# Performance work log

Measured on AMD Instinct MI355X. Metric: run time of the kernel, lower is better.

## Reference

```python
import jax, jax.numpy as jnp
import numpy as np

S, B, E, H = 2048, 4, 512, 8
HD = E // H


def setup_inputs() -> dict:
    key = jax.random.key(0)
    ks = jax.random.split(key, 5)
    scale = 1.0 / np.sqrt(E)
    return {
        "query": jax.random.normal(ks[0], (S, B, E), jnp.float32),
        "key": jax.random.normal(ks[1], (S, B, E), jnp.float32),
        "value": jax.random.normal(ks[2], (S, B, E), jnp.float32),
        "in_proj_weight": jax.random.normal(ks[3], (3 * E, E), jnp.float32) * scale,
        "in_proj_bias": jnp.zeros((3 * E,), jnp.float32),
        "out_proj_weight": jax.random.normal(ks[4], (E, E), jnp.float32) * scale,
        "out_proj_bias": jnp.zeros((E,), jnp.float32),
    }


def reference(query, key, value, in_proj_weight, in_proj_bias, out_proj_weight, out_proj_bias):
    tgt_len, bsz, embed_dim = query.shape
    src_len = key.shape[0]
    # Quirk of this module: first chunk (w_qk) projects BOTH q and k; third chunk projects v.
    w_qk = in_proj_weight[:embed_dim]
    w_v = in_proj_weight[2 * embed_dim:]
    b_qk = in_proj_bias[:embed_dim]
    b_v = in_proj_bias[2 * embed_dim:]
    q = query @ w_qk.T + b_qk          # [S, B, E]
    k = key @ w_qk.T + b_qk
    v = value @ w_v.T + b_v
    # (S, B, E) -> (B*H, S, HD)
    def split_heads(x, n):
        return x.reshape(n, bsz * H, HD).transpose(1, 0, 2)
    q = split_heads(q, tgt_len) / jnp.sqrt(jnp.asarray(HD, q.dtype))
    k = split_heads(k, src_len)
    v = split_heads(v, src_len)
    scores = jnp.einsum("bqd,bkd->bqk", q, k)          # [B*H, S, S] full score matrix
    attn = jax.nn.softmax(scores, axis=-1)
    out = jnp.einsum("bqk,bkd->bqd", attn, v)          # [B*H, S, HD]
    out = out.transpose(1, 0, 2).reshape(tgt_len * bsz, embed_dim)
    out = out @ out_proj_weight.T + out_proj_bias
    return out.reshape(tgt_len, bsz, embed_dim)
```

## Files before the change

kernel.cpp:

```cpp
#include <hip/hip_runtime.h>
#include <hip/hip_bf16.h>

typedef __attribute__((ext_vector_type(8))) short s16x8;
typedef __attribute__((ext_vector_type(4))) short s16x4;
typedef __attribute__((ext_vector_type(4))) float f32x4;

#if __has_builtin(__builtin_amdgcn_exp2f)
#define EXP2F(x) __builtin_amdgcn_exp2f(x)
#else
#define EXP2F(x) exp2f(x)
#endif

#define S_LEN 2048
#define EMB   512
#define MROWS 8192

__device__ __forceinline__ float bf2f(short x) {
    union { float f; unsigned u; } z; z.u = ((unsigned)(unsigned short)x) << 16; return z.f;
}
__device__ __forceinline__ short f2bf(float f) {
    union { float f; unsigned u; } z; z.f = f;
    unsigned r = z.u + 0x7FFF + ((z.u >> 16) & 1);
    return (short)(r >> 16);
}
__device__ __forceinline__ short f2bf_fast(float f) {
    union { float f; unsigned u; } z; z.f = f;
    return (short)((z.u + 0x8000u) >> 16);
}

template<int AF32, int BF32>
__device__ __forceinline__ void gemm_mainloop(const void* __restrict__ Ag,
                                              const void* __restrict__ Bg,
                                              short* sA, short* sB,
                                              f32x4 acc[2][4], int K)
{
    const int tid  = threadIdx.x;
    const int lane = tid & 63;
    const int wv   = tid >> 6;
    const int l15  = lane & 15, quad = lane >> 4;
    const int wm   = (wv >> 1) * 32, wn = (wv & 1) * 64;

    f32x4 afr[2], bfr[2];
    s16x8 ahr, bhr;

    auto loadT = [&](const void* G, int kt, f32x4* fr, s16x8& hr, int F32) {
        if (F32) {
#pragma unroll
            for (int p = 0; p < 2; ++p) {
                int c = tid + p * 512;
                fr[p] = *(const f32x4*)((const float*)G + (size_t)(c >> 3) * K + kt + (c & 7) * 4);
            }
        } else {
            hr = *(const s16x8*)((const short*)G + (size_t)(tid >> 2) * K + kt + (tid & 3) * 8);
        }
    };
    auto commitT = [&](short* s, f32x4* fr, s16x8& hr, int F32) {
        if (F32) {
#pragma unroll
            for (int p = 0; p < 2; ++p) {
                int c = tid + p * 512;
                s16x4 o4;
                o4[0] = f2bf_fast(fr[p][0]); o4[1] = f2bf_fast(fr[p][1]);
                o4[2] = f2bf_fast(fr[p][2]); o4[3] = f2bf_fast(fr[p][3]);
                *(s16x4*)(s + c * 4) = o4;
            }
        } else {
            *(s16x8*)(s + tid * 8) = hr;
        }
    };

    loadT(Ag, 0, afr, ahr, AF32);
    loadT(Bg, 0, bfr, bhr, BF32);
    commitT(sA, afr, ahr, AF32);
    commitT(sB, bfr, bhr, BF32);
    __syncthreads();

    int cur = 0;
    for (int kt = 0; kt < K; kt += 32) {
        const int ktn = (kt + 32 < K) ? kt + 32 : 0;
        loadT(Ag, ktn, afr, ahr, AF32);
        loadT(Bg, ktn, bfr, bhr, BF32);

        const short* sAc = sA + cur * 4096;
        const short* sBc = sB + cur * 4096;
        s16x8 aF[2], bF[4];
#pragma unroll
        for (int i = 0; i < 2; ++i)
            aF[i] = *(const s16x8*)(sAc + (wm + i * 16 + l15) * 32 + quad * 8);
#pragma unroll
        for (int j = 0; j < 4; ++j)
            bF[j] = *(const s16x8*)(sBc + (wn + j * 16 + l15) * 32 + quad * 8);
#pragma unroll
        for (int i = 0; i < 2; ++i)
#pragma unroll
            for (int j = 0; j < 4; ++j)
                acc[i][j] = __builtin_amdgcn_mfma_f32_16x16x32_bf16(aF[i], bF[j], acc[i][j], 0, 0, 0);

        commitT(sA + (cur ^ 1) * 4096, afr, ahr, AF32);
        commitT(sB + (cur ^ 1) * 4096, bfr, bhr, BF32);
        __syncthreads();
        cur ^= 1;
    }
}

__global__ __launch_bounds__(512, 4) void qkv_proj(const float* __restrict__ query,
                                                   const float* __restrict__ key,
                                                   const float* __restrict__ value,
                                                   const float* __restrict__ W,
                                                   const float* __restrict__ bias,
                                                   short* __restrict__ q,
                                                   short* __restrict__ k,
                                                   short* __restrict__ vt)
{
    __shared__ __align__(16) short smem[16384];
    short* sA = smem;
    short* sB = smem + 8192;

    const int z = blockIdx.z;
    const float* X  = (z == 0) ? query : (z == 1) ? key : value;
    const float* Wz = W    + (z == 2 ? (size_t)1024 * EMB : 0);
    const float* bz = bias + (z == 2 ? 1024 : 0);
    const float scale = (z == 0) ? 0.125f * 1.44269504f : 1.0f;

    const int blockM = blockIdx.x * 128, blockN = blockIdx.y * 128;

    f32x4 acc[2][4];
#pragma unroll
    for (int i = 0; i < 2; ++i)
#pragma unroll
        for (int j = 0; j < 4; ++j)
            acc[i][j] = (f32x4){0.f, 0.f, 0.f, 0.f};

    gemm_mainloop<1, 1>(X + (size_t)blockM * EMB, Wz + (size_t)blockN * EMB,
                        sA, sB, acc, EMB);

    const int tid = threadIdx.x, lane = tid & 63, wv = tid >> 6;
    const int l15 = lane & 15, quad = lane >> 4;
    const int wm = (wv >> 1) * 32, wn = (wv & 1) * 64;

#pragma unroll
    for (int j = 0; j < 4; ++j) {
        int colL = wn + j * 16 + l15;
        float bval = bz[blockN + colL];
        int hL = colL >> 6, hd = colL & 63;
#pragma unroll
        for (int i = 0; i < 2; ++i) {
#pragma unroll
            for (int r = 0; r < 4; ++r) {
                int rowL = wm + i * 16 + quad * 4 + r;
                int b = rowL & 3, sp = rowL >> 2;
                float val = (acc[i][j][r] + bval) * scale;
                int idx = (z == 2) ? (((b * 2 + hL) * 64 + hd) * 32 + sp)
                                   : (((b * 2 + hL) * 32 + sp) * 64 + hd);
                smem[idx] = f2bf(val);
            }
        }
    }
    __syncthreads();

    const s16x8* src = (const s16x8*)(smem + tid * 32);
    if (z == 2) {
        int b = tid >> 7, hL = (tid >> 6) & 1, hd = tid & 63;
        int h = (blockN >> 6) + hL;
        short* dst = vt + ((size_t)(b * 8 + h) * 64 + hd) * 2048 + (blockM >> 2);
#pragma unroll
        for (int u = 0; u < 4; ++u) ((s16x8*)dst)[u] = src[u];
    } else {
        int b = tid >> 7, hL = (tid >> 6) & 1;
        int sp = (tid >> 1) & 31, hdh = (tid & 1) * 32;
        int h = (blockN >> 6) + hL;
        short* dstp = (z == 0) ? q : k;
        short* dst = dstp + ((size_t)(b * 8 + h) * 2048 + (blockM >> 2) + sp) * 64 + hdh;
#pragma unroll
        for (int u = 0; u < 4; ++u) ((s16x8*)dst)[u] = src[u];
    }
}

__global__ __launch_bounds__(256, 2) void flash_attn(const short* __restrict__ q,
                                                     const short* __restrict__ k,
                                                     const short* __restrict__ vt,
                                                     short* __restrict__ attn)
{
    __shared__ __align__(16) short sK[2][64 * 72];
    __shared__ __align__(16) short sV[2][64 * 72];
    const int bh = blockIdx.x;
    const int q0 = blockIdx.y * 128;
    const int tid = threadIdx.x, wv = tid >> 6, lane = tid & 63;
    const int l15 = lane & 15, quad = lane >> 4;

    s16x8 qf[2][2];
#pragma unroll
    for (int qr = 0; qr < 2; ++qr) {
        const short* qp = q + ((size_t)(bh * 2048 + q0 + wv * 32 + qr * 16 + l15)) * 64 + quad * 8;
        qf[qr][0] = *(const s16x8*)qp;
        qf[qr][1] = *(const s16x8*)(qp + 32);
    }

    const short* kg = k  + (size_t)bh * 2048 * 64;
    const short* vg = vt + (size_t)bh * 64 * 2048;

    const int r0 = tid >> 3,          c0 = (tid & 7) * 8;
    const int r1 = (tid + 256) >> 3,  c1 = ((tid + 256) & 7) * 8;
    const int p0 = (r0 & 35) | ((r0 & 24) >> 1) | ((r0 & 4) << 2);
    const int p1 = (r1 & 35) | ((r1 & 24) >> 1) | ((r1 & 4) << 2);

    f32x4 o[2][4];
    float ls[2][4];
#pragma unroll
    for (int qr = 0; qr < 2; ++qr)
#pragma unroll
        for (int i = 0; i < 4; ++i) { o[qr][i] = (f32x4){0.f, 0.f, 0.f, 0.f}; ls[qr][i] = 0.f; }

    s16x8 ka = *(const s16x8*)(kg + (size_t)r0 * 64 + c0);
    s16x8 kb = *(const s16x8*)(kg + (size_t)r1 * 64 + c1);
    s16x8 va = *(const s16x8*)(vg + (size_t)r0 * 2048 + c0);
    s16x8 vb = *(const s16x8*)(vg + (size_t)r1 * 2048 + c1);
    *(s16x8*)(sK[0] + p0 * 72 + c0) = ka;
    *(s16x8*)(sK[0] + p1 * 72 + c1) = kb;
    *(s16x8*)(sV[0] + r0 * 72 + c0) = va;
    *(s16x8*)(sV[0] + r1 * 72 + c1) = vb;
    __syncthreads();

    int cur = 0;
    for (int kt = 0; kt < 2048; kt += 64) {
        const int ktn = (kt + 64) & 2047;
        ka = *(const s16x8*)(kg + (size_t)(ktn + r0) * 64 + c0);
        kb = *(const s16x8*)(kg + (size_t)(ktn + r1) * 64 + c1);
        va = *(const s16x8*)(vg + (size_t)r0 * 2048 + ktn + c0);
        vb = *(const s16x8*)(vg + (size_t)r1 * 2048 + ktn + c1);

        const short* Kc = sK[cur];
        const short* Vc = sV[cur];

        f32x4 sc[2][4];
#pragma unroll
        for (int ct = 0; ct < 4; ++ct) {
            s16x8 kf0 = *(const s16x8*)(Kc + (ct * 16 + l15) * 72 + quad * 8);
            s16x8 kf1 = *(const s16x8*)(Kc + (ct * 16 + l15) * 72 + quad * 8 + 32);
#pragma unroll
            for (int qr = 0; qr < 2; ++qr) {
                f32x4 c = (f32x4){0.f, 0.f, 0.f, 0.f};
                c = __builtin_amdgcn_mfma_f32_16x16x32_bf16(kf0, qf[qr][0], c, 0, 0, 0);
                c = __builtin_amdgcn_mfma_f32_16x16x32_bf16(kf1, qf[qr][1], c, 0, 0, 0);
                sc[qr][ct] = c;
            }
        }
        s16x8 pf[2][2];
#pragma unroll
        for (int qr = 0; qr < 2; ++qr)
#pragma unroll
            for (int c = 0; c < 2; ++c)
#pragma unroll
                for (int h = 0; h < 2; ++h)
#pragma unroll
                    for (int r = 0; r < 4; ++r) {
                        float p = EXP2F(sc[qr][2 * c + h][r]);
                        ls[qr][r] += p;
                        pf[qr][c][h * 4 + r] = f2bf_fast(p);
                    }
#pragma unroll
        for (int nt = 0; nt < 4; ++nt)
#pragma unroll
            for (int c = 0; c < 2; ++c) {
                s16x8 vf = *(const s16x8*)(Vc + (nt * 16 + l15) * 72 + c * 32 + quad * 8);
#pragma unroll
                for (int qr = 0; qr < 2; ++qr)
                    o[qr][nt] = __builtin_amdgcn_mfma_f32_16x16x32_bf16(pf[qr][c], vf, o[qr][nt], 0, 0, 0);
            }
        short* Kn = sK[cur ^ 1];
        short* Vn = sV[cur ^ 1];
        *(s16x8*)(Kn + p0 * 72 + c0) = ka;
        *(s16x8*)(Kn + p1 * 72 + c1) = kb;
        *(s16x8*)(Vn + r0 * 72 + c0) = va;
        *(s16x8*)(Vn + r1 * 72 + c1) = vb;
        __syncthreads();
        cur ^= 1;
    }

    const int b = bh >> 3, h = bh & 7;
#pragma unroll
    for (int qr = 0; qr < 2; ++qr) {
        float s = ls[qr][0] + ls[qr][1] + ls[qr][2] + ls[qr][3];
        s += __shfl_xor(s, 16, 64);
        s += __shfl_xor(s, 32, 64);
        float sinv = 1.0f / s;
        float inv[4];
#pragma unroll
        for (int r = 0; r < 4; ++r)
            inv[r] = __shfl(sinv, quad * 20 + r, 64);
#pragma unroll
        for (int r = 0; r < 4; ++r) {
            int srow = q0 + wv * 32 + qr * 16 + quad * 4 + r;
#pragma unroll
            for (int nt = 0; nt < 4; ++nt)
                attn[(size_t)(srow * 4 + b) * 512 + h * 64 + nt * 16 + l15] = f2bf(o[qr][nt][r] * inv[r]);
        }
    }
}

__global__ __launch_bounds__(512, 4) void out_proj(const short* __restrict__ attn,
                                                   const float* __restrict__ W,
                                                   const float* __restrict__ bias,
                                                   float* __restrict__ out)
{
    __shared__ __align__(16) short sA[2 * 4096], sB[2 * 4096];
    const int blockM = blockIdx.x * 128, blockN = blockIdx.y * 128;

    f32x4 acc[2][4];
#pragma unroll
    for (int i = 0; i < 2; ++i)
#pragma unroll
        for (int j = 0; j < 4; ++j)
            acc[i][j] = (f32x4){0.f, 0.f, 0.f, 0.f};

    gemm_mainloop<0, 1>(attn + (size_t)blockM * EMB, W + (size_t)blockN * EMB,
                        sA, sB, acc, EMB);

    const int tid = threadIdx.x, lane = tid & 63, wv = tid >> 6;
    const int l15 = lane & 15, quad = lane >> 4;
    const int wm = (wv >> 1) * 32, wn = (wv & 1) * 64;

#pragma unroll
    for (int j = 0; j < 4; ++j) {
        int col = blockN + wn + j * 16 + l15;
        float bval = bias[col];
#pragma unroll
        for (int i = 0; i < 2; ++i) {
#pragma unroll
            for (int r = 0; r < 4; ++r) {
                int row = blockM + wm + i * 16 + quad * 4 + r;
                out[(size_t)row * 512 + col] = acc[i][j][r] + bval;
            }
        }
    }
}

extern "C" void kernel_launch(void* const* d_in, const int* in_sizes, int n_in,
                              void* d_out, int out_size, void* d_ws, size_t ws_size,
                              hipStream_t stream)
{
    const float* query = (const float*)d_in[0];
    const float* key   = (const float*)d_in[1];
    const float* value = (const float*)d_in[2];
    const float* ipw   = (const float*)d_in[3];
    const float* ipb   = (const float*)d_in[4];
    const float* opw   = (const float*)d_in[5];
    const float* opb   = (const float*)d_in[6];
    float* out = (float*)d_out;

    const size_t NELEM = (size_t)MROWS * EMB;
    short* q    = (short*)d_ws;
    short* k    = q + NELEM;
    short* attn = k + NELEM;
    short* vt   = (short*)d_out;

    qkv_proj  <<<dim3(64, 4, 3), 512, 0, stream>>>(query, key, value, ipw, ipb, q, k, vt);
    flash_attn<<<dim3(32, 16),   256, 0, stream>>>(q, k, vt, attn);
    out_proj  <<<dim3(64, 4),    512, 0, stream>>>(attn, opw, opb, out);
}
```

Baseline: 188.0 us.

## Pre-convert weights to bf16 and store LDS tiles in MFMA fragment order

Adds a small kernel that converts the input projection weight to bf16 once per call, so the QKV GEMM reads half the bytes for its B operand and skips per-tile conversion. The GEMM and flash-attention staging are reorganised so each thread writes LDS data already in MFMA fragment order. Fragment reads then become contiguous 16-byte per-lane loads with no padding or swizzle arithmetic. The cost is an extra kernel launch, and the weight copy lives in scratch space carved from the output buffer.

After: 204.9 us. 9.0% more time.

```diff
diff --git a/kernel.cpp b/kernel.cpp
--- a/kernel.cpp
+++ b/kernel.cpp
@@ -28,6 +28,20 @@
     return (short)((z.u + 0x8000u) >> 16);
 }
 
+__global__ __launch_bounds__(256) void w_to_bf16(const float* __restrict__ W,
+                                                 short* __restrict__ wb, int n)
+{
+    int i = (blockIdx.x * 256 + threadIdx.x) * 8;
+    if (i < n) {
+        f32x4 a = *(const f32x4*)(W + i);
+        f32x4 b = *(const f32x4*)(W + i + 4);
+        s16x8 o;
+        o[0] = f2bf(a[0]); o[1] = f2bf(a[1]); o[2] = f2bf(a[2]); o[3] = f2bf(a[3]);
+        o[4] = f2bf(b[0]); o[5] = f2bf(b[1]); o[6] = f2bf(b[2]); o[7] = f2bf(b[3]);
+        *(s16x8*)(wb + i) = o;
+    }
+}
+
 template<int AF32, int BF32>
 __device__ __forceinline__ void gemm_mainloop(const void* __restrict__ Ag,
                                               const void* __restrict__ Bg,
@@ -37,33 +51,33 @@
     const int tid  = threadIdx.x;
     const int lane = tid & 63;
     const int wv   = tid >> 6;
-    const int l15  = lane & 15, quad = lane >> 4;
-    const int wm   = (wv >> 1) * 32, wn = (wv & 1) * 64;
+
+    const int srow = (tid >> 6) * 16 + (tid & 15);
+    const int scol = ((tid >> 4) & 3) * 8;
+
+    const int amt = (wv >> 1) * 2;
+    const int bnt = (wv & 1) * 4;
 
     f32x4 afr[2], bfr[2];
     s16x8 ahr, bhr;
 
     auto loadT = [&](const void* G, int kt, f32x4* fr, s16x8& hr, int F32) {
         if (F32) {
-#pragma unroll
-            for (int p = 0; p < 2; ++p) {
-                int c = tid + p * 512;
-                fr[p] = *(const f32x4*)((const float*)G + (size_t)(c >> 3) * K + kt + (c & 7) * 4);
-            }
+            const float* g = (const float*)G + (size_t)srow * K + kt + scol;
+            fr[0] = *(const f32x4*)g;
+            fr[1] = *(const f32x4*)(g + 4);
         } else {
-            hr = *(const s16x8*)((const short*)G + (size_t)(tid >> 2) * K + kt + (tid & 3) * 8);
+            hr = *(const s16x8*)((const short*)G + (size_t)srow * K + kt + scol);
         }
     };
     auto commitT = [&](short* s, f32x4* fr, s16x8& hr, int F32) {
         if (F32) {
-#pragma unroll
-            for (int p = 0; p < 2; ++p) {
-                int c = tid + p * 512;
-                s16x4 o4;
-                o4[0] = f2bf_fast(fr[p][0]); o4[1] = f2bf_fast(fr[p][1]);
-                o4[2] = f2bf_fast(fr[p][2]); o4[3] = f2bf_fast(fr[p][3]);
-                *(s16x4*)(s + c * 4) = o4;
-            }
+            s16x8 o;
+            o[0] = f2bf_fast(fr[0][0]); o[1] = f2bf_fast(fr[0][1]);
+            o[2] = f2bf_fast(fr[0][2]); o[3] = f2bf_fast(fr[0][3]);
+            o[4] = f2bf_fast(fr[1][0]); o[5] = f2bf_fast(fr[1][1]);
+            o[6] = f2bf_fast(fr[1][2]); o[7] = f2bf_fast(fr[1][3]);
+            *(s16x8*)(s + tid * 8) = o;
         } else {
             *(s16x8*)(s + tid * 8) = hr;
         }
@@ -86,10 +100,10 @@
         s16x8 aF[2], bF[4];
 #pragma unroll
         for (int i = 0; i < 2; ++i)
-            aF[i] = *(const s16x8*)(sAc + (wm + i * 16 + l15) * 32 + quad * 8);
+            aF[i] = *(const s16x8*)(sAc + ((amt + i) * 64 + lane) * 8);
 #pragma unroll
         for (int j = 0; j < 4; ++j)
-            bF[j] = *(const s16x8*)(sBc + (wn + j * 16 + l15) * 32 + quad * 8);
+            bF[j] = *(const s16x8*)(sBc + ((bnt + j) * 64 + lane) * 8);
 #pragma unroll
         for (int i = 0; i < 2; ++i)
 #pragma unroll
@@ -106,7 +120,7 @@
 __global__ __launch_bounds__(512, 4) void qkv_proj(const float* __restrict__ query,
                                                    const float* __restrict__ key,
                                                    const float* __restrict__ value,
-                                                   const float* __restrict__ W,
+                                                   const short* __restrict__ wb,
                                                    const float* __restrict__ bias,
                                                    short* __restrict__ q,
                                                    short* __restrict__ k,
@@ -118,7 +132,7 @@
 
     const int z = blockIdx.z;
     const float* X  = (z == 0) ? query : (z == 1) ? key : value;
-    const float* Wz = W    + (z == 2 ? (size_t)1024 * EMB : 0);
+    const short* Wz = wb   + (z == 2 ? (size_t)1024 * EMB : 0);
     const float* bz = bias + (z == 2 ? 1024 : 0);
     const float scale = (z == 0) ? 0.125f * 1.44269504f : 1.0f;
 
@@ -131,7 +145,7 @@
         for (int j = 0; j < 4; ++j)
             acc[i][j] = (f32x4){0.f, 0.f, 0.f, 0.f};
 
-    gemm_mainloop<1, 1>(X + (size_t)blockM * EMB, Wz + (size_t)blockN * EMB,
+    gemm_mainloop<1, 0>(X + (size_t)blockM * EMB, Wz + (size_t)blockN * EMB,
                         sA, sB, acc, EMB);
 
     const int tid = threadIdx.x, lane = tid & 63, wv = tid >> 6;
@@ -181,8 +195,8 @@
                                                      const short* __restrict__ vt,
                                                      short* __restrict__ attn)
 {
-    __shared__ __align__(16) short sK[2][64 * 72];
-    __shared__ __align__(16) short sV[2][64 * 72];
+    __shared__ __align__(16) short sK[2][4096];
+    __shared__ __align__(16) short sV[2][4096];
     const int bh = blockIdx.x;
     const int q0 = blockIdx.y * 128;
     const int tid = threadIdx.x, wv = tid >> 6, lane = tid & 63;
@@ -199,10 +213,14 @@
     const short* kg = k  + (size_t)bh * 2048 * 64;
     const short* vg = vt + (size_t)bh * 64 * 2048;
 
-    const int r0 = tid >> 3,          c0 = (tid & 7) * 8;
-    const int r1 = (tid + 256) >> 3,  c1 = ((tid + 256) & 7) * 8;
-    const int p0 = (r0 & 35) | ((r0 & 24) >> 1) | ((r0 & 4) << 2);
-    const int p1 = (r1 & 35) | ((r1 & 24) >> 1) | ((r1 & 4) << 2);
+    const int l15s = tid & 15;
+    const int qs   = (tid >> 4) & 3;
+    const int cts  = tid >> 6;
+    const int pr   = cts * 16 + l15s;
+    const int rK   = (pr & 35) | ((pr & 12) << 1) | ((pr & 16) >> 2);
+    const int hdV  = cts * 16 + l15s;
+    const short* kgt = kg + (size_t)rK * 64 + qs * 8;
+    const short* vgt = vg + (size_t)hdV * 2048 + qs * 8;
 
     f32x4 o[2][4];
     float ls[2][4];
@@ -211,23 +229,23 @@
 #pragma unroll
         for (int i = 0; i < 4; ++i) { o[qr][i] = (f32x4){0.f, 0.f, 0.f, 0.f}; ls[qr][i] = 0.f; }
 
-    s16x8 ka = *(const s16x8*)(kg + (size_t)r0 * 64 + c0);
-    s16x8 kb = *(const s16x8*)(kg + (size_t)r1 * 64 + c1);
-    s16x8 va = *(const s16x8*)(vg + (size_t)r0 * 2048 + c0);
-    s16x8 vb = *(const s16x8*)(vg + (size_t)r1 * 2048 + c1);
-    *(s16x8*)(sK[0] + p0 * 72 + c0) = ka;
-    *(s16x8*)(sK[0] + p1 * 72 + c1) = kb;
-    *(s16x8*)(sV[0] + r0 * 72 + c0) = va;
-    *(s16x8*)(sV[0] + r1 * 72 + c1) = vb;
+    s16x8 ka = *(const s16x8*)(kgt);
+    s16x8 kb = *(const s16x8*)(kgt + 32);
+    s16x8 va = *(const s16x8*)(vgt);
+    s16x8 vb = *(const s16x8*)(vgt + 32);
+    *(s16x8*)(sK[0] + tid * 8)        = ka;
+    *(s16x8*)(sK[0] + 2048 + tid * 8) = kb;
+    *(s16x8*)(sV[0] + tid * 8)        = va;
+    *(s16x8*)(sV[0] + 2048 + tid * 8) = vb;
     __syncthreads();
 
     int cur = 0;
     for (int kt = 0; kt < 2048; kt += 64) {
         const int ktn = (kt + 64) & 2047;
-        ka = *(const s16x8*)(kg + (size_t)(ktn + r0) * 64 + c0);
-        kb = *(const s16x8*)(kg + (size_t)(ktn + r1) * 64 + c1);
-        va = *(const s16x8*)(vg + (size_t)r0 * 2048 + ktn + c0);
-        vb = *(const s16x8*)(vg + (size_t)r1 * 2048 + ktn + c1);
+        ka = *(const s16x8*)(kgt + (size_t)ktn * 64);
+        kb = *(const s16x8*)(kgt + (size_t)ktn * 64 + 32);
+        va = *(const s16x8*)(vgt + ktn);
+        vb = *(const s16x8*)(vgt + ktn + 32);
 
         const short* Kc = sK[cur];
         const short* Vc = sV[cur];
@@ -235,8 +253,8 @@
         f32x4 sc[2][4];
 #pragma unroll
         for (int ct = 0; ct < 4; ++ct) {
-            s16x8 kf0 = *(const s16x8*)(Kc + (ct * 16 + l15) * 72 + quad * 8);
-            s16x8 kf1 = *(const s16x8*)(Kc + (ct * 16 + l15) * 72 + quad * 8 + 32);
+            s16x8 kf0 = *(const s16x8*)(Kc + (ct * 64 + lane) * 8);
+            s16x8 kf1 = *(const s16x8*)(Kc + (ct * 64 + lane) * 8 + 2048);
 #pragma unroll
             for (int qr = 0; qr < 2; ++qr) {
                 f32x4 c = (f32x4){0.f, 0.f, 0.f, 0.f};
@@ -262,17 +280,15 @@
         for (int nt = 0; nt < 4; ++nt)
 #pragma unroll
             for (int c = 0; c < 2; ++c) {
-                s16x8 vf = *(const s16x8*)(Vc + (nt * 16 + l15) * 72 + c * 32 + quad * 8);
+                s16x8 vf = *(const s16x8*)(Vc + ((c * 4 + nt) * 64 + lane) * 8);
 #pragma unroll
                 for (int qr = 0; qr < 2; ++qr)
                     o[qr][nt] = __builtin_amdgcn_mfma_f32_16x16x32_bf16(pf[qr][c], vf, o[qr][nt], 0, 0, 0);
             }
-        short* Kn = sK[cur ^ 1];
-        short* Vn = sV[cur ^ 1];
-        *(s16x8*)(Kn + p0 * 72 + c0) = ka;
-        *(s16x8*)(Kn + p1 * 72 + c1) = kb;
-        *(s16x8*)(Vn + r0 * 72 + c0) = va;
-        *(s16x8*)(Vn + r1 * 72 + c1) = vb;
+        *(s16x8*)(sK[cur ^ 1] + tid * 8)        = ka;
+        *(s16x8*)(sK[cur ^ 1] + 2048 + tid * 8) = kb;
+        *(s16x8*)(sV[cur ^ 1] + tid * 8)        = va;
+        *(s16x8*)(sV[cur ^ 1] + 2048 + tid * 8) = vb;
         __syncthreads();
         cur ^= 1;
     }
@@ -353,8 +369,10 @@
     short* k    = q + NELEM;
     short* attn = k + NELEM;
     short* vt   = (short*)d_out;
-
-    qkv_proj  <<<dim3(64, 4, 3), 512, 0, stream>>>(query, key, value, ipw, ipb, q, k, vt);
+    short* wb   = (short*)d_out + NELEM;
+
+    w_to_bf16 <<<dim3(384),      256, 0, stream>>>(ipw, wb, 1536 * EMB);
+    qkv_proj  <<<dim3(64, 4, 3), 512, 0, stream>>>(query, key, value, wb, ipb, q, k, vt);
     flash_attn<<<dim3(32, 16),   256, 0, stream>>>(q, k, vt, attn);
     out_proj  <<<dim3(64, 4),    512, 0, stream>>>(attn, opw, opb, out);
 }
```

## Swizzle LDS layouts into MFMA fragment order to avoid bank conflicts

Applied to the files above, without the earlier changes.

Shared-memory tiles in the projection GEMM mainloop and the flash-attention K/V buffers are re-laid out in MFMA fragment order with an XOR swizzle, so each lane reads its 16-byte fragment at a contiguous swizzled offset instead of a padded row-major stride. The V-transpose staging buffer in the QKV epilogue also gets an XOR swizzle on its column chunks. The aim is to remove LDS bank conflicts on fragment reads and writes, and in attention to drop the padding, which shrinks LDS use. Global load patterns change as well (fewer rows per thread, two strided chunks), which may affect coalescing.

Result: slower. 202.9 us (+7.9%).

```diff
diff --git a/kernel.cpp b/kernel.cpp
--- a/kernel.cpp
+++ b/kernel.cpp
@@ -15,9 +15,6 @@
 #define EMB   512
 #define MROWS 8192
 
-__device__ __forceinline__ float bf2f(short x) {
-    union { float f; unsigned u; } z; z.u = ((unsigned)(unsigned short)x) << 16; return z.f;
-}
 __device__ __forceinline__ short f2bf(float f) {
     union { float f; unsigned u; } z; z.f = f;
     unsigned r = z.u + 0x7FFF + ((z.u >> 16) & 1);
@@ -27,6 +24,7 @@
     union { float f; unsigned u; } z; z.f = f;
     return (short)((z.u + 0x8000u) >> 16);
 }
+__device__ __forceinline__ int swzs(int s) { return s ^ ((s >> 3) & 7); }
 
 template<int AF32, int BF32>
 __device__ __forceinline__ void gemm_mainloop(const void* __restrict__ Ag,
@@ -37,35 +35,39 @@
     const int tid  = threadIdx.x;
     const int lane = tid & 63;
     const int wv   = tid >> 6;
-    const int l15  = lane & 15, quad = lane >> 4;
-    const int wm   = (wv >> 1) * 32, wn = (wv & 1) * 64;
+    const int lsw  = lane ^ ((lane >> 3) & 7);
+    const int amt  = (wv >> 1) * 2;
+    const int bnt  = (wv & 1) * 4;
+
+    const int brow = tid >> 2, bqd = tid & 3;
+    const int boff = swzs((brow >> 4) * 64 + bqd * 16 + (brow & 15)) * 8;
+    const int frow = tid >> 3, ffc = tid & 7;
+    const int foff = swzs((frow >> 4) * 64 + (ffc >> 1) * 16 + (frow & 15)) * 8
+                   + (ffc & 1) * 4;
 
     f32x4 afr[2], bfr[2];
     s16x8 ahr, bhr;
 
     auto loadT = [&](const void* G, int kt, f32x4* fr, s16x8& hr, int F32) {
         if (F32) {
-#pragma unroll
-            for (int p = 0; p < 2; ++p) {
-                int c = tid + p * 512;
-                fr[p] = *(const f32x4*)((const float*)G + (size_t)(c >> 3) * K + kt + (c & 7) * 4);
-            }
+            const float* g = (const float*)G + (size_t)frow * K + kt + ffc * 4;
+            fr[0] = *(const f32x4*)g;
+            fr[1] = *(const f32x4*)(g + (size_t)64 * K);
         } else {
-            hr = *(const s16x8*)((const short*)G + (size_t)(tid >> 2) * K + kt + (tid & 3) * 8);
+            hr = *(const s16x8*)((const short*)G + (size_t)brow * K + kt + bqd * 8);
         }
     };
     auto commitT = [&](short* s, f32x4* fr, s16x8& hr, int F32) {
         if (F32) {
 #pragma unroll
             for (int p = 0; p < 2; ++p) {
-                int c = tid + p * 512;
                 s16x4 o4;
                 o4[0] = f2bf_fast(fr[p][0]); o4[1] = f2bf_fast(fr[p][1]);
                 o4[2] = f2bf_fast(fr[p][2]); o4[3] = f2bf_fast(fr[p][3]);
-                *(s16x4*)(s + c * 4) = o4;
+                *(s16x4*)(s + foff + p * 2048) = o4;
             }
         } else {
-            *(s16x8*)(s + tid * 8) = hr;
+            *(s16x8*)(s + boff) = hr;
         }
     };
 
@@ -86,10 +88,10 @@
         s16x8 aF[2], bF[4];
 #pragma unroll
         for (int i = 0; i < 2; ++i)
-            aF[i] = *(const s16x8*)(sAc + (wm + i * 16 + l15) * 32 + quad * 8);
+            aF[i] = *(const s16x8*)(sAc + ((amt + i) * 64 + lsw) * 8);
 #pragma unroll
         for (int j = 0; j < 4; ++j)
-            bF[j] = *(const s16x8*)(sBc + (wn + j * 16 + l15) * 32 + quad * 8);
+            bF[j] = *(const s16x8*)(sBc + ((bnt + j) * 64 + lsw) * 8);
 #pragma unroll
         for (int i = 0; i < 2; ++i)
 #pragma unroll
@@ -150,22 +152,29 @@
                 int rowL = wm + i * 16 + quad * 4 + r;
                 int b = rowL & 3, sp = rowL >> 2;
                 float val = (acc[i][j][r] + bval) * scale;
-                int idx = (z == 2) ? (((b * 2 + hL) * 64 + hd) * 32 + sp)
-                                   : (((b * 2 + hL) * 32 + sp) * 64 + hd);
+                int idx;
+                if (z == 2) {
+                    int R = (b * 2 + hL) * 64 + hd;
+                    idx = R * 32 + (((sp >> 3) ^ (R & 3)) << 3) + (sp & 7);
+                } else {
+                    idx = ((b * 2 + hL) * 32 + sp) * 64 + hd;
+                }
                 smem[idx] = f2bf(val);
             }
         }
     }
     __syncthreads();
 
-    const s16x8* src = (const s16x8*)(smem + tid * 32);
     if (z == 2) {
+        int R = tid;
         int b = tid >> 7, hL = (tid >> 6) & 1, hd = tid & 63;
         int h = (blockN >> 6) + hL;
         short* dst = vt + ((size_t)(b * 8 + h) * 64 + hd) * 2048 + (blockM >> 2);
 #pragma unroll
-        for (int u = 0; u < 4; ++u) ((s16x8*)dst)[u] = src[u];
+        for (int u = 0; u < 4; ++u)
+            ((s16x8*)dst)[u] = *(const s16x8*)(smem + R * 32 + ((u ^ (R & 3)) << 3));
     } else {
+        const s16x8* src = (const s16x8*)(smem + tid * 32);
         int b = tid >> 7, hL = (tid >> 6) & 1;
         int sp = (tid >> 1) & 31, hdh = (tid & 1) * 32;
         int h = (blockN >> 6) + hL;
@@ -181,12 +190,13 @@
                                                      const short* __restrict__ vt,
                                                      short* __restrict__ attn)
 {
-    __shared__ __align__(16) short sK[2][64 * 72];
-    __shared__ __align__(16) short sV[2][64 * 72];
+    __shared__ __align__(16) short sK[2][4096];
+    __shared__ __align__(16) short sV[2][4096];
     const int bh = blockIdx.x;
     const int q0 = blockIdx.y * 128;
     const int tid = threadIdx.x, wv = tid >> 6, lane = tid & 63;
     const int l15 = lane & 15, quad = lane >> 4;
+    const int lsw = lane ^ ((lane >> 3) & 7);
 
     s16x8 qf[2][2];
 #pragma unroll
@@ -199,10 +209,12 @@
     const short* kg = k  + (size_t)bh * 2048 * 64;
     const short* vg = vt + (size_t)bh * 64 * 2048;
 
-    const int r0 = tid >> 3,          c0 = (tid & 7) * 8;
-    const int r1 = (tid + 256) >> 3,  c1 = ((tid + 256) & 7) * 8;
-    const int p0 = (r0 & 35) | ((r0 & 24) >> 1) | ((r0 & 4) << 2);
-    const int p1 = (r1 & 35) | ((r1 & 24) >> 1) | ((r1 & 4) << 2);
+    const int rk = tid >> 2, qd = tid & 3;
+    const int pr = (rk & 35) | ((rk & 24) >> 1) | ((rk & 4) << 2);
+    const int kw0 = swzs((pr >> 4) * 64 + qd * 16 + (pr & 15)) * 8;
+    const int vw0 = swzs((rk >> 4) * 64 + qd * 16 + (rk & 15)) * 8;
+    const short* kgt = kg + (size_t)rk * 64 + qd * 8;
+    const short* vgt = vg + (size_t)rk * 2048 + qd * 8;
 
     f32x4 o[2][4];
     float ls[2][4];
@@ -211,23 +223,23 @@
 #pragma unroll
         for (int i = 0; i < 4; ++i) { o[qr][i] = (f32x4){0.f, 0.f, 0.f, 0.f}; ls[qr][i] = 0.f; }
 
-    s16x8 ka = *(const s16x8*)(kg + (size_t)r0 * 64 + c0);
-    s16x8 kb = *(const s16x8*)(kg + (size_t)r1 * 64 + c1);
-    s16x8 va = *(const s16x8*)(vg + (size_t)r0 * 2048 + c0);
-    s16x8 vb = *(const s16x8*)(vg + (size_t)r1 * 2048 + c1);
-    *(s16x8*)(sK[0] + p0 * 72 + c0) = ka;
-    *(s16x8*)(sK[0] + p1 * 72 + c1) = kb;
-    *(s16x8*)(sV[0] + r0 * 72 + c0) = va;
-    *(s16x8*)(sV[0] + r1 * 72 + c1) = vb;
+    s16x8 ka = *(const s16x8*)(kgt);
+    s16x8 kb = *(const s16x8*)(kgt + 32);
+    s16x8 va = *(const s16x8*)(vgt);
+    s16x8 vb = *(const s16x8*)(vgt + 32);
+    *(s16x8*)(sK[0] + kw0)        = ka;
+    *(s16x8*)(sK[0] + kw0 + 2048) = kb;
+    *(s16x8*)(sV[0] + vw0)        = va;
+    *(s16x8*)(sV[0] + vw0 + 2048) = vb;
     __syncthreads();
 
     int cur = 0;
     for (int kt = 0; kt < 2048; kt += 64) {
         const int ktn = (kt + 64) & 2047;
-        ka = *(const s16x8*)(kg + (size_t)(ktn + r0) * 64 + c0);
-        kb = *(const s16x8*)(kg + (size_t)(ktn + r1) * 64 + c1);
-        va = *(const s16x8*)(vg + (size_t)r0 * 2048 + ktn + c0);
-        vb = *(const s16x8*)(vg + (size_t)r1 * 2048 + ktn + c1);
+        ka = *(const s16x8*)(kgt + (size_t)ktn * 64);
+        kb = *(const s16x8*)(kgt + (size_t)ktn * 64 + 32);
+        va = *(const s16x8*)(vgt + ktn);
+        vb = *(const s16x8*)(vgt + ktn + 32);
 
         const short* Kc = sK[cur];
         const short* Vc = sV[cur];
@@ -235,8 +247,8 @@
         f32x4 sc[2][4];
 #pragma unroll
         for (int ct = 0; ct < 4; ++ct) {
-            s16x8 kf0 = *(const s16x8*)(Kc + (ct * 16 + l15) * 72 + quad * 8);
-            s16x8 kf1 = *(const s16x8*)(Kc + (ct * 16 + l15) * 72 + quad * 8 + 32);
+            s16x8 kf0 = *(const s16x8*)(Kc + (ct * 64 + lsw) * 8);
+            s16x8 kf1 = *(const s16x8*)(Kc + (ct * 64 + lsw) * 8 + 2048);
 #pragma unroll
             for (int qr = 0; qr < 2; ++qr) {
                 f32x4 c = (f32x4){0.f, 0.f, 0.f, 0.f};
@@ -262,17 +274,15 @@
         for (int nt = 0; nt < 4; ++nt)
 #pragma unroll
             for (int c = 0; c < 2; ++c) {
-                s16x8 vf = *(const s16x8*)(Vc + (nt * 16 + l15) * 72 + c * 32 + quad * 8);
+                s16x8 vf = *(const s16x8*)(Vc + ((c * 4 + nt) * 64 + lsw) * 8);
 #pragma unroll
                 for (int qr = 0; qr < 2; ++qr)
                     o[qr][nt] = __builtin_amdgcn_mfma_f32_16x16x32_bf16(pf[qr][c], vf, o[qr][nt], 0, 0, 0);
             }
-        short* Kn = sK[cur ^ 1];
-        short* Vn = sV[cur ^ 1];
-        *(s16x8*)(Kn + p0 * 72 + c0) = ka;
-        *(s16x8*)(Kn + p1 * 72 + c1) = kb;
-        *(s16x8*)(Vn + r0 * 72 + c0) = va;
-        *(s16x8*)(Vn + r1 * 72 + c1) = vb;
+        *(s16x8*)(sK[cur ^ 1] + kw0)        = ka;
+        *(s16x8*)(sK[cur ^ 1] + kw0 + 2048) = kb;
+        *(s16x8*)(sV[cur ^ 1] + vw0)        = va;
+        *(s16x8*)(sV[cur ^ 1] + vw0 + 2048) = vb;
         __syncthreads();
         cur ^= 1;
     }
```
